# Performance work log

Measured on AMD Instinct MI355X. Metric: run time of the kernel, lower is better.

## Reference

```python
import jax, jax.numpy as jnp
import numpy as np

TOP_K = 2  # num_experts_per_tok


def setup_inputs() -> dict:
    key = jax.random.key(0)
    k1, k2, k3, k4, k5 = jax.random.split(key, 5)
    B, S, D, F, E = 2, 1024, 1024, 2048, 8
    return {
        "x": jax.random.normal(k1, (B, S, D), dtype=jnp.float32),
        "router_kernel_DE": jax.random.normal(k2, (D, E), dtype=jnp.float32) * 0.02,
        "kernel_gating_EDF": jax.random.normal(k3, (E, D, F), dtype=jnp.float32) * 0.02,
        "kernel_up_EDF": jax.random.normal(k4, (E, D, F), dtype=jnp.float32) * 0.02,
        "kernel_down_EFD": jax.random.normal(k5, (E, F, D), dtype=jnp.float32) * 0.02,
    }


def reference(x, router_kernel_DE, kernel_gating_EDF, kernel_up_EDF, kernel_down_EFD):
    E = router_kernel_DE.shape[-1]
    x = x.astype(jnp.float32)
    # --- Router ---
    logits_BSE = jnp.einsum('BSD,DE->BSE', x, router_kernel_DE)
    probs_BSE = jax.nn.softmax(logits_BSE.astype(jnp.float32), axis=-1)
    weights_BSK, indices_BSK = jax.lax.top_k(probs_BSE, TOP_K)
    norm_weights_BSK = jax.nn.softmax(weights_BSK, axis=-1)
    # scatter top-k weights into dense [B,S,E]
    one_hot_BSKE = jax.nn.one_hot(indices_BSK, num_classes=E, dtype=x.dtype)
    full_weights_BSE = jnp.sum(one_hot_BSKE * norm_weights_BSK[..., None], axis=2)
    # --- Dense-over-all-experts MoE forward ---
    gating_BSEF = jnp.einsum('BSD,EDF->BSEF', x, kernel_gating_EDF)
    act_BSEF = jax.nn.silu(gating_BSEF)
    up_BSEF = jnp.einsum('BSD,EDF->BSEF', x, kernel_up_EDF)
    fuse_BSEF = act_BSEF * up_BSEF
    down_BSED = jnp.einsum('BSEF,EFD->BSED', fuse_BSEF, kernel_down_EFD)
    out_BSD = jnp.einsum('BSED,BSE->BSD', down_BSED, full_weights_BSE)
    return out_BSD.astype(jnp.float32)
```

## Files before the change

### kernel.cpp

```cpp
#include <hip/hip_runtime.h>
#include <hip/hip_bf16.h>
#include <stdint.h>

#define T_TOK 2048
#define DIM 1024
#define FDIM 2048
#define NEXP 8
#define NSLOT 4096
#define MAXTILE 64

typedef short bf16x8 __attribute__((ext_vector_type(8)));
typedef float f32x4 __attribute__((ext_vector_type(4)));

__device__ __forceinline__ unsigned short f2bf(float f) {
  union { float f; unsigned int u; } v; v.f = f;
  unsigned int r = v.u + 0x7FFFu + ((v.u >> 16) & 1u);
  return (unsigned short)(r >> 16);
}

__device__ __forceinline__ void gld_lds16(const void* g, void* l) {
  __builtin_amdgcn_global_load_lds(
      (const __attribute__((address_space(1))) unsigned int*)g,
      (__attribute__((address_space(3))) unsigned int*)l, 16, 0, 0);
}

__global__ void router_kernel(const float* __restrict__ x, const float* __restrict__ rk,
                              int* __restrict__ counts, int* __restrict__ tok_e,
                              float* __restrict__ tok_w) {
  int w = threadIdx.x >> 6, lane = threadIdx.x & 63;
  int t = blockIdx.x * 4 + w;
  float acc[NEXP];
#pragma unroll
  for (int e = 0; e < NEXP; ++e) acc[e] = 0.f;
  const float4* xr = (const float4*)(x + (size_t)t * DIM);
#pragma unroll
  for (int i = 0; i < 4; ++i) {
    float4 xv = xr[i * 64 + lane];
    int d0 = (i * 64 + lane) * 4;
#pragma unroll
    for (int j = 0; j < 4; ++j) {
      const float4* rr = (const float4*)(rk + (size_t)(d0 + j) * NEXP);
      float4 r0 = rr[0], r1 = rr[1];
      float xs = (j == 0) ? xv.x : (j == 1) ? xv.y : (j == 2) ? xv.z : xv.w;
      acc[0] += xs * r0.x; acc[1] += xs * r0.y; acc[2] += xs * r0.z; acc[3] += xs * r0.w;
      acc[4] += xs * r1.x; acc[5] += xs * r1.y; acc[6] += xs * r1.z; acc[7] += xs * r1.w;
    }
  }
#pragma unroll
  for (int off = 32; off > 0; off >>= 1) {
#pragma unroll
    for (int e = 0; e < NEXP; ++e) acc[e] += __shfl_xor(acc[e], off, 64);
  }
  if (lane == 0) {
    float m = acc[0];
    for (int e = 1; e < NEXP; ++e) m = fmaxf(m, acc[e]);
    float p[NEXP], s = 0.f;
    for (int e = 0; e < NEXP; ++e) { p[e] = expf(acc[e] - m); s += p[e]; }
    float inv = 1.f / s;
    for (int e = 0; e < NEXP; ++e) p[e] *= inv;
    int i1 = 0;
    for (int e = 1; e < NEXP; ++e) if (p[e] > p[i1]) i1 = e;
    int i2 = (i1 == 0) ? 1 : 0;
    for (int e = 0; e < NEXP; ++e) if (e != i1 && p[e] > p[i2]) i2 = e;
    float e1 = expf(p[i1]), e2 = expf(p[i2]);
    float winv = 1.f / (e1 + e2);
    tok_e[t * 2] = i1; tok_e[t * 2 + 1] = i2;
    tok_w[t * 2] = e1 * winv; tok_w[t * 2 + 1] = e2 * winv;
    atomicAdd(&counts[i1], 1); atomicAdd(&counts[i2], 1);
  }
}

__global__ void scan_kernel(const int* __restrict__ counts, int* __restrict__ offsets,
                            int* __restrict__ tile_e, int* __restrict__ tile_mt,
                            int* __restrict__ ntiles) {
  if (threadIdx.x == 0) {
    int s = 0, t = 0;
    for (int e = 0; e < NEXP; ++e) {
      offsets[e] = s; s += counts[e];
      int nt = (counts[e] + 127) >> 7;
      for (int m = 0; m < nt; ++m) { tile_e[t] = e; tile_mt[t] = m; ++t; }
    }
    ntiles[0] = t;
  }
}

__global__ void assign_kernel(const int* __restrict__ tok_e, const float* __restrict__ tok_w,
                              const int* __restrict__ offsets, int* __restrict__ cursor,
                              int* __restrict__ slot_token, float* __restrict__ slot_weight,
                              int* __restrict__ tok_slot) {
  int t = blockIdx.x * 256 + threadIdx.x;
  if (t >= T_TOK) return;
#pragma unroll
  for (int k = 0; k < 2; ++k) {
    int e = tok_e[t * 2 + k];
    int pos = atomicAdd(&cursor[e], 1);
    int slot = offsets[e] + pos;
    slot_token[slot] = t;
    slot_weight[slot] = tok_w[t * 2 + k];
    tok_slot[t * 2 + k] = slot;
  }
}

__global__ void cvt_x_kernel(const float* __restrict__ x, unsigned short* __restrict__ xb) {
  int i = blockIdx.x * 256 + threadIdx.x;
  const float4* p = (const float4*)x;
  float4 a = p[i * 2], b = p[i * 2 + 1];
  uint4 o;
  o.x = ((unsigned)f2bf(a.y) << 16) | f2bf(a.x);
  o.y = ((unsigned)f2bf(a.w) << 16) | f2bf(a.z);
  o.z = ((unsigned)f2bf(b.y) << 16) | f2bf(b.x);
  o.w = ((unsigned)f2bf(b.w) << 16) | f2bf(b.z);
  ((uint4*)xb)[i] = o;
}

__global__ void transpose_cvt_kernel(const float* __restrict__ in, unsigned short* __restrict__ out,
                                     int R, int C) {
  __shared__ float lds[64][65];
  int e = blockIdx.z;
  size_t base = (size_t)e * (size_t)R * (size_t)C;
  int rb = blockIdx.y * 64, cb = blockIdx.x * 64;
  int tid = threadIdx.x;
  int col4 = (tid & 15) * 4, row = tid >> 4;
#pragma unroll
  for (int it = 0; it < 4; ++it) {
    int r = row + it * 16;
    float4 v = *(const float4*)(in + base + (size_t)(rb + r) * C + cb + col4);
    lds[col4 + 0][r] = v.x; lds[col4 + 1][r] = v.y;
    lds[col4 + 2][r] = v.z; lds[col4 + 3][r] = v.w;
  }
  __syncthreads();
  int r2 = (tid & 31) * 2, c = tid >> 5;
#pragma unroll
  for (int it = 0; it < 8; ++it) {
    int cc = c + it * 8;
    unsigned v = ((unsigned)f2bf(lds[cc][r2 + 1]) << 16) | f2bf(lds[cc][r2]);
    *(unsigned*)(out + base + (size_t)(cb + cc) * R + rb + r2) = v;
  }
}


__global__ __launch_bounds__(256) void gemm_gateup(
    const unsigned short* __restrict__ xb, const unsigned short* __restrict__ wg,
    const unsigned short* __restrict__ wu, const int* __restrict__ counts,
    const int* __restrict__ offsets, const int* __restrict__ slot_token,
    const int* __restrict__ tile_e, const int* __restrict__ tile_mt,
    const int* __restrict__ ntiles, unsigned short* __restrict__ fuse) {
  int ys = blockIdx.y;
  if (ys >= ntiles[0]) return;
  int e = tile_e[ys], mt = tile_mt[ys];
  int cnt = counts[e];
  int off = offsets[e];
  int nt = blockIdx.x;
  __shared__ unsigned short Al[128 * 64];
  __shared__ unsigned short Bgl[128 * 64];
  __shared__ unsigned short Bul[128 * 64];
  int tid = threadIdx.x, w = tid >> 6, lane = tid & 63;
  int w4 = w * 4;
  int csrc = ((lane & 7) ^ (lane >> 3)) * 8;
  const unsigned short* asrc[4];
  const unsigned short* bgsrc[4];
  const unsigned short* busrc[4];
#pragma unroll
  for (int ii = 0; ii < 4; ++ii) {
    int i = w4 + ii;
    int r = i * 8 + (lane >> 3);
    int row = mt * 128 + r;
    int tok = (row < cnt) ? slot_token[off + row] : 0;
    asrc[ii] = xb + (size_t)tok * DIM + csrc;
    size_t frow = (size_t)e * FDIM + (size_t)(nt * 128 + r);
    bgsrc[ii] = wg + frow * DIM + csrc;
    busrc[ii] = wu + frow * DIM + csrc;
  }
  f32x4 accg[4][4] = {};
  f32x4 accu[4][4] = {};
  int wr = (w >> 1) * 64, wc = (w & 1) * 64;
  int swz = (lane & 7) << 3;
  int kof0 = ((lane >> 4) * 8) ^ swz;
  int kof1 = (32 + (lane >> 4) * 8) ^ swz;
  for (int k0 = 0; k0 < DIM; k0 += 64) {
#pragma unroll
    for (int ii = 0; ii < 4; ++ii) {
      int i = w4 + ii;
      gld_lds16(asrc[ii] + k0, &Al[i * 512]);
      gld_lds16(bgsrc[ii] + k0, &Bgl[i * 512]);
      gld_lds16(busrc[ii] + k0, &Bul[i * 512]);
    }
    __syncthreads();
#pragma unroll
    for (int kk = 0; kk < 2; ++kk) {
      int kof = kk ? kof1 : kof0;
      bf16x8 af[4], bg[4], bu[4];
#pragma unroll
      for (int q = 0; q < 4; ++q) {
        af[q] = *(const bf16x8*)&Al[(wr + q * 16 + (lane & 15)) * 64 + kof];
        bg[q] = *(const bf16x8*)&Bgl[(wc + q * 16 + (lane & 15)) * 64 + kof];
        bu[q] = *(const bf16x8*)&Bul[(wc + q * 16 + (lane & 15)) * 64 + kof];
      }
#pragma unroll
      for (int m4 = 0; m4 < 4; ++m4) {
#pragma unroll
        for (int n4 = 0; n4 < 4; ++n4) {
          accg[m4][n4] = __builtin_amdgcn_mfma_f32_16x16x32_bf16(af[m4], bg[n4], accg[m4][n4], 0, 0, 0);
          accu[m4][n4] = __builtin_amdgcn_mfma_f32_16x16x32_bf16(af[m4], bu[n4], accu[m4][n4], 0, 0, 0);
        }
      }
    }
    __syncthreads();
  }
#pragma unroll
  for (int m4 = 0; m4 < 4; ++m4) {
#pragma unroll
    for (int n4 = 0; n4 < 4; ++n4) {
      f32x4 g = accg[m4][n4], u = accu[m4][n4];
#pragma unroll
      for (int j = 0; j < 4; ++j) {
        int r = wr + m4 * 16 + (lane >> 4) * 4 + j;
        int row = mt * 128 + r;
        if (row < cnt) {
          float gv = g[j];
          float val = gv / (1.f + expf(-gv)) * u[j];
          int f = nt * 128 + wc + n4 * 16 + (lane & 15);
          fuse[(size_t)(off + row) * FDIM + f] = f2bf(val);
        }
      }
    }
  }
}

__global__ __launch_bounds__(256) void gemm_down(
    const unsigned short* __restrict__ fuse, const unsigned short* __restrict__ wd,
    const int* __restrict__ counts, const int* __restrict__ offsets,
    const float* __restrict__ slot_weight, const int* __restrict__ tile_e,
    const int* __restrict__ tile_mt, const int* __restrict__ ntiles,
    float* __restrict__ part) {
  int ys = blockIdx.y;
  if (ys >= ntiles[0]) return;
  int e = tile_e[ys], mt = tile_mt[ys];
  int cnt = counts[e];
  int off = offsets[e];
  int nt = blockIdx.x;
  __shared__ unsigned short Al[128 * 64];
  __shared__ unsigned short Bl[128 * 64];
  int tid = threadIdx.x, w = tid >> 6, lane = tid & 63;
  int w4 = w * 4;
  int csrc = ((lane & 7) ^ (lane >> 3)) * 8;
  const unsigned short* asrc[4];
  const unsigned short* bsrc[4];
#pragma unroll
  for (int ii = 0; ii < 4; ++ii) {
    int i = w4 + ii;
    int r = i * 8 + (lane >> 3);
    int row = mt * 128 + r;
    int grow = (row < cnt) ? (off + row) : off;
    asrc[ii] = fuse + (size_t)grow * FDIM + csrc;
    size_t drow = (size_t)e * DIM + (size_t)(nt * 128 + r);
    bsrc[ii] = wd + drow * FDIM + csrc;
  }
  f32x4 acc[4][4] = {};
  int wr = (w >> 1) * 64, wc = (w & 1) * 64;
  int swz = (lane & 7) << 3;
  int kof0 = ((lane >> 4) * 8) ^ swz;
  int kof1 = (32 + (lane >> 4) * 8) ^ swz;
  for (int k0 = 0; k0 < FDIM; k0 += 64) {
#pragma unroll
    for (int ii = 0; ii < 4; ++ii) {
      int i = w4 + ii;
      gld_lds16(asrc[ii] + k0, &Al[i * 512]);
      gld_lds16(bsrc[ii] + k0, &Bl[i * 512]);
    }
    __syncthreads();
#pragma unroll
    for (int kk = 0; kk < 2; ++kk) {
      int kof = kk ? kof1 : kof0;
      bf16x8 af[4], bfr[4];
#pragma unroll
      for (int q = 0; q < 4; ++q) {
        af[q] = *(const bf16x8*)&Al[(wr + q * 16 + (lane & 15)) * 64 + kof];
        bfr[q] = *(const bf16x8*)&Bl[(wc + q * 16 + (lane & 15)) * 64 + kof];
      }
#pragma unroll
      for (int m4 = 0; m4 < 4; ++m4) {
#pragma unroll
        for (int n4 = 0; n4 < 4; ++n4) {
          acc[m4][n4] = __builtin_amdgcn_mfma_f32_16x16x32_bf16(af[m4], bfr[n4], acc[m4][n4], 0, 0, 0);
        }
      }
    }
    __syncthreads();
  }
#pragma unroll
  for (int m4 = 0; m4 < 4; ++m4) {
#pragma unroll
    for (int j = 0; j < 4; ++j) {
      int r = wr + m4 * 16 + (lane >> 4) * 4 + j;
      int row = mt * 128 + r;
      if (row < cnt) {
        float wgt = slot_weight[off + row];
#pragma unroll
        for (int n4 = 0; n4 < 4; ++n4) {
          int d = nt * 128 + wc + n4 * 16 + (lane & 15);
          part[(size_t)(off + row) * DIM + d] = acc[m4][n4][j] * wgt;
        }
      }
    }
  }
}

__global__ void combine_kernel(const float* __restrict__ part, const int* __restrict__ tok_slot,
                               float* __restrict__ out) {
  int i = blockIdx.x * 256 + threadIdx.x;
  int t = i >> 8;
  int c = i & 255;
  int s0 = tok_slot[t * 2], s1 = tok_slot[t * 2 + 1];
  float4 a = ((const float4*)(part + (size_t)s0 * DIM))[c];
  float4 b = ((const float4*)(part + (size_t)s1 * DIM))[c];
  float4 o;
  o.x = a.x + b.x; o.y = a.y + b.y; o.z = a.z + b.z; o.w = a.w + b.w;
  ((float4*)(out + (size_t)t * DIM))[c] = o;
}

extern "C" void kernel_launch(void* const* d_in, const int* in_sizes, int n_in,
                              void* d_out, int out_size, void* d_ws, size_t ws_size,
                              hipStream_t stream) {
  (void)in_sizes; (void)n_in; (void)out_size;
  const float* x    = (const float*)d_in[0];
  const float* rk   = (const float*)d_in[1];
  const float* wg_f = (const float*)d_in[2];
  const float* wu_f = (const float*)d_in[3];
  const float* wd_f = (const float*)d_in[4];
  float* out = (float*)d_out;

  char* ws = (char*)d_ws;
  size_t o_xb   = 0;
  size_t o_wg   = o_xb + (size_t)T_TOK * DIM * 2;
  size_t o_wu   = o_wg + (size_t)NEXP * FDIM * DIM * 2;
  size_t o_wd   = o_wu + (size_t)NEXP * FDIM * DIM * 2;
  size_t o_fuse = o_wd + (size_t)NEXP * DIM * FDIM * 2;
  size_t o_part = o_fuse + (size_t)NSLOT * FDIM * 2;
  size_t o_meta = o_part + (size_t)NSLOT * DIM * 4;
  size_t o_counts = o_meta;
  size_t o_cursor = o_counts + 32;
  size_t o_offs   = o_cursor + 32;
  size_t o_tok_e  = o_offs + 32;
  size_t o_tok_w  = o_tok_e + (size_t)T_TOK * 2 * 4;
  size_t o_tok_s  = o_tok_w + (size_t)T_TOK * 2 * 4;
  size_t o_st     = o_tok_s + (size_t)T_TOK * 2 * 4;
  size_t o_sw     = o_st + (size_t)NSLOT * 4;
  size_t o_te     = o_sw + (size_t)NSLOT * 4;
  size_t o_tm     = o_te + MAXTILE * 4;
  size_t o_ntl    = o_tm + MAXTILE * 4;
  size_t need     = o_ntl + 32;
  if (ws_size < need) return;

  unsigned short* xb   = (unsigned short*)(ws + o_xb);
  unsigned short* wgt  = (unsigned short*)(ws + o_wg);
  unsigned short* wut  = (unsigned short*)(ws + o_wu);
  unsigned short* wdt  = (unsigned short*)(ws + o_wd);
  unsigned short* fuse = (unsigned short*)(ws + o_fuse);
  float* part          = (float*)(ws + o_part);
  int* counts          = (int*)(ws + o_counts);
  int* cursor          = (int*)(ws + o_cursor);
  int* offsets         = (int*)(ws + o_offs);
  int* tok_e           = (int*)(ws + o_tok_e);
  float* tok_w         = (float*)(ws + o_tok_w);
  int* tok_slot        = (int*)(ws + o_tok_s);
  int* slot_token      = (int*)(ws + o_st);
  float* slot_weight   = (float*)(ws + o_sw);
  int* tile_e          = (int*)(ws + o_te);
  int* tile_mt         = (int*)(ws + o_tm);
  int* ntiles          = (int*)(ws + o_ntl);

  hipMemsetAsync(ws + o_counts, 0, 64, stream);
  router_kernel<<<T_TOK / 4, 256, 0, stream>>>(x, rk, counts, tok_e, tok_w);
  scan_kernel<<<1, 64, 0, stream>>>(counts, offsets, tile_e, tile_mt, ntiles);
  assign_kernel<<<T_TOK / 256, 256, 0, stream>>>(tok_e, tok_w, offsets, cursor,
                                                 slot_token, slot_weight, tok_slot);
  cvt_x_kernel<<<(T_TOK * DIM / 8) / 256, 256, 0, stream>>>(x, xb);
  transpose_cvt_kernel<<<dim3(FDIM / 64, DIM / 64, NEXP), 256, 0, stream>>>(wg_f, wgt, DIM, FDIM);
  transpose_cvt_kernel<<<dim3(FDIM / 64, DIM / 64, NEXP), 256, 0, stream>>>(wu_f, wut, DIM, FDIM);
  transpose_cvt_kernel<<<dim3(DIM / 64, FDIM / 64, NEXP), 256, 0, stream>>>(wd_f, wdt, FDIM, DIM);
  gemm_gateup<<<dim3(FDIM / 128, MAXTILE * 40 / 64, 1), 256, 0, stream>>>(
      xb, wgt, wut, counts, offsets, slot_token, tile_e, tile_mt, ntiles, fuse);
  gemm_down<<<dim3(DIM / 128, MAXTILE * 40 / 64, 1), 256, 0, stream>>>(
      fuse, wdt, counts, offsets, slot_weight, tile_e, tile_mt, ntiles, part);
  combine_kernel<<<(T_TOK * DIM / 4) / 256, 256, 0, stream>>>(part, tok_slot, out);
}
```

Measured before the change: 290.4 us.

## Narrow GEMM N-tiles, split-K the down projection, store partials in bf16

Halves the N tile width of both expert GEMMs from 128 to 64 and splits the down-projection K dimension into two halves via a z grid dimension. The goal is more workgroups to fill the GPU's compute units and better occupancy through launch bounds hints. Split-K partials are written as bf16 into a doubled buffer and summed in the combine kernel, which now reads four bf16 vectors per output. Narrower tiles cut arithmetic intensity and re-read the A tile more often, and bf16 partials add rounding error.

```diff
diff --git a/kernel.cpp b/kernel.cpp
--- a/kernel.cpp
+++ b/kernel.cpp
@@ -10,12 +10,18 @@
 #define MAXTILE 64
 
 typedef short bf16x8 __attribute__((ext_vector_type(8)));
+typedef unsigned short u16x8 __attribute__((ext_vector_type(8)));
 typedef float f32x4 __attribute__((ext_vector_type(4)));
 
 __device__ __forceinline__ unsigned short f2bf(float f) {
   union { float f; unsigned int u; } v; v.f = f;
   unsigned int r = v.u + 0x7FFFu + ((v.u >> 16) & 1u);
   return (unsigned short)(r >> 16);
+}
+
+__device__ __forceinline__ float bf2f(unsigned short x) {
+  union { unsigned int u; float f; } v; v.u = ((unsigned int)x) << 16;
+  return v.f;
 }
 
 __device__ __forceinline__ void gld_lds16(const void* g, void* l) {
@@ -139,7 +145,7 @@
 }
 
 
-__global__ __launch_bounds__(256) void gemm_gateup(
+__global__ __launch_bounds__(256, 4) void gemm_gateup(
     const unsigned short* __restrict__ xb, const unsigned short* __restrict__ wg,
     const unsigned short* __restrict__ wu, const int* __restrict__ counts,
     const int* __restrict__ offsets, const int* __restrict__ slot_token,
@@ -152,54 +158,59 @@
   int off = offsets[e];
   int nt = blockIdx.x;
   __shared__ unsigned short Al[128 * 64];
-  __shared__ unsigned short Bgl[128 * 64];
-  __shared__ unsigned short Bul[128 * 64];
+  __shared__ unsigned short Bgl[64 * 64];
+  __shared__ unsigned short Bul[64 * 64];
   int tid = threadIdx.x, w = tid >> 6, lane = tid & 63;
-  int w4 = w * 4;
   int csrc = ((lane & 7) ^ (lane >> 3)) * 8;
   const unsigned short* asrc[4];
-  const unsigned short* bgsrc[4];
-  const unsigned short* busrc[4];
+  const unsigned short* bgsrc[2];
+  const unsigned short* busrc[2];
 #pragma unroll
   for (int ii = 0; ii < 4; ++ii) {
-    int i = w4 + ii;
-    int r = i * 8 + (lane >> 3);
+    int r = (w * 4 + ii) * 8 + (lane >> 3);
     int row = mt * 128 + r;
     int tok = (row < cnt) ? slot_token[off + row] : 0;
     asrc[ii] = xb + (size_t)tok * DIM + csrc;
-    size_t frow = (size_t)e * FDIM + (size_t)(nt * 128 + r);
+  }
+#pragma unroll
+  for (int ii = 0; ii < 2; ++ii) {
+    int r = (w * 2 + ii) * 8 + (lane >> 3);
+    size_t frow = (size_t)e * FDIM + (size_t)(nt * 64 + r);
     bgsrc[ii] = wg + frow * DIM + csrc;
     busrc[ii] = wu + frow * DIM + csrc;
   }
-  f32x4 accg[4][4] = {};
-  f32x4 accu[4][4] = {};
-  int wr = (w >> 1) * 64, wc = (w & 1) * 64;
+  f32x4 accg[4][2] = {};
+  f32x4 accu[4][2] = {};
+  int wr = (w >> 1) * 64, wc = (w & 1) * 32;
   int swz = (lane & 7) << 3;
   int kof0 = ((lane >> 4) * 8) ^ swz;
   int kof1 = (32 + (lane >> 4) * 8) ^ swz;
   for (int k0 = 0; k0 < DIM; k0 += 64) {
 #pragma unroll
-    for (int ii = 0; ii < 4; ++ii) {
-      int i = w4 + ii;
-      gld_lds16(asrc[ii] + k0, &Al[i * 512]);
-      gld_lds16(bgsrc[ii] + k0, &Bgl[i * 512]);
-      gld_lds16(busrc[ii] + k0, &Bul[i * 512]);
+    for (int ii = 0; ii < 4; ++ii)
+      gld_lds16(asrc[ii] + k0, &Al[(w * 4 + ii) * 512]);
+#pragma unroll
+    for (int ii = 0; ii < 2; ++ii) {
+      gld_lds16(bgsrc[ii] + k0, &Bgl[(w * 2 + ii) * 512]);
+      gld_lds16(busrc[ii] + k0, &Bul[(w * 2 + ii) * 512]);
     }
     __syncthreads();
 #pragma unroll
     for (int kk = 0; kk < 2; ++kk) {
       int kof = kk ? kof1 : kof0;
-      bf16x8 af[4], bg[4], bu[4];
-#pragma unroll
-      for (int q = 0; q < 4; ++q) {
+      bf16x8 af[4], bg[2], bu[2];
+#pragma unroll
+      for (int q = 0; q < 4; ++q)
         af[q] = *(const bf16x8*)&Al[(wr + q * 16 + (lane & 15)) * 64 + kof];
+#pragma unroll
+      for (int q = 0; q < 2; ++q) {
         bg[q] = *(const bf16x8*)&Bgl[(wc + q * 16 + (lane & 15)) * 64 + kof];
         bu[q] = *(const bf16x8*)&Bul[(wc + q * 16 + (lane & 15)) * 64 + kof];
       }
 #pragma unroll
       for (int m4 = 0; m4 < 4; ++m4) {
 #pragma unroll
-        for (int n4 = 0; n4 < 4; ++n4) {
+        for (int n4 = 0; n4 < 2; ++n4) {
           accg[m4][n4] = __builtin_amdgcn_mfma_f32_16x16x32_bf16(af[m4], bg[n4], accg[m4][n4], 0, 0, 0);
           accu[m4][n4] = __builtin_amdgcn_mfma_f32_16x16x32_bf16(af[m4], bu[n4], accu[m4][n4], 0, 0, 0);
         }
@@ -210,7 +221,7 @@
 #pragma unroll
   for (int m4 = 0; m4 < 4; ++m4) {
 #pragma unroll
-    for (int n4 = 0; n4 < 4; ++n4) {
+    for (int n4 = 0; n4 < 2; ++n4) {
       f32x4 g = accg[m4][n4], u = accu[m4][n4];
 #pragma unroll
       for (int j = 0; j < 4; ++j) {
@@ -219,7 +230,7 @@
         if (row < cnt) {
           float gv = g[j];
           float val = gv / (1.f + expf(-gv)) * u[j];
-          int f = nt * 128 + wc + n4 * 16 + (lane & 15);
+          int f = nt * 64 + wc + n4 * 16 + (lane & 15);
           fuse[(size_t)(off + row) * FDIM + f] = f2bf(val);
         }
       }
@@ -227,61 +238,66 @@
   }
 }
 
-__global__ __launch_bounds__(256) void gemm_down(
+__global__ __launch_bounds__(256, 4) void gemm_down(
     const unsigned short* __restrict__ fuse, const unsigned short* __restrict__ wd,
     const int* __restrict__ counts, const int* __restrict__ offsets,
     const float* __restrict__ slot_weight, const int* __restrict__ tile_e,
     const int* __restrict__ tile_mt, const int* __restrict__ ntiles,
-    float* __restrict__ part) {
+    unsigned short* __restrict__ part2) {
   int ys = blockIdx.y;
   if (ys >= ntiles[0]) return;
   int e = tile_e[ys], mt = tile_mt[ys];
   int cnt = counts[e];
   int off = offsets[e];
   int nt = blockIdx.x;
+  int z = blockIdx.z;
+  int kbase = z * (FDIM / 2);
   __shared__ unsigned short Al[128 * 64];
-  __shared__ unsigned short Bl[128 * 64];
+  __shared__ unsigned short Bl[64 * 64];
   int tid = threadIdx.x, w = tid >> 6, lane = tid & 63;
-  int w4 = w * 4;
   int csrc = ((lane & 7) ^ (lane >> 3)) * 8;
   const unsigned short* asrc[4];
-  const unsigned short* bsrc[4];
+  const unsigned short* bsrc[2];
 #pragma unroll
   for (int ii = 0; ii < 4; ++ii) {
-    int i = w4 + ii;
-    int r = i * 8 + (lane >> 3);
+    int r = (w * 4 + ii) * 8 + (lane >> 3);
     int row = mt * 128 + r;
     int grow = (row < cnt) ? (off + row) : off;
-    asrc[ii] = fuse + (size_t)grow * FDIM + csrc;
-    size_t drow = (size_t)e * DIM + (size_t)(nt * 128 + r);
-    bsrc[ii] = wd + drow * FDIM + csrc;
-  }
-  f32x4 acc[4][4] = {};
-  int wr = (w >> 1) * 64, wc = (w & 1) * 64;
+    asrc[ii] = fuse + (size_t)grow * FDIM + kbase + csrc;
+  }
+#pragma unroll
+  for (int ii = 0; ii < 2; ++ii) {
+    int r = (w * 2 + ii) * 8 + (lane >> 3);
+    size_t drow = (size_t)e * DIM + (size_t)(nt * 64 + r);
+    bsrc[ii] = wd + drow * FDIM + kbase + csrc;
+  }
+  f32x4 acc[4][2] = {};
+  int wr = (w >> 1) * 64, wc = (w & 1) * 32;
   int swz = (lane & 7) << 3;
   int kof0 = ((lane >> 4) * 8) ^ swz;
   int kof1 = (32 + (lane >> 4) * 8) ^ swz;
-  for (int k0 = 0; k0 < FDIM; k0 += 64) {
-#pragma unroll
-    for (int ii = 0; ii < 4; ++ii) {
-      int i = w4 + ii;
-      gld_lds16(asrc[ii] + k0, &Al[i * 512]);
-      gld_lds16(bsrc[ii] + k0, &Bl[i * 512]);
-    }
+  for (int k0 = 0; k0 < FDIM / 2; k0 += 64) {
+#pragma unroll
+    for (int ii = 0; ii < 4; ++ii)
+      gld_lds16(asrc[ii] + k0, &Al[(w * 4 + ii) * 512]);
+#pragma unroll
+    for (int ii = 0; ii < 2; ++ii)
+      gld_lds16(bsrc[ii] + k0, &Bl[(w * 2 + ii) * 512]);
     __syncthreads();
 #pragma unroll
     for (int kk = 0; kk < 2; ++kk) {
       int kof = kk ? kof1 : kof0;
-      bf16x8 af[4], bfr[4];
-#pragma unroll
-      for (int q = 0; q < 4; ++q) {
+      bf16x8 af[4], bfr[2];
+#pragma unroll
+      for (int q = 0; q < 4; ++q)
         af[q] = *(const bf16x8*)&Al[(wr + q * 16 + (lane & 15)) * 64 + kof];
+#pragma unroll
+      for (int q = 0; q < 2; ++q)
         bfr[q] = *(const bf16x8*)&Bl[(wc + q * 16 + (lane & 15)) * 64 + kof];
-      }
 #pragma unroll
       for (int m4 = 0; m4 < 4; ++m4) {
 #pragma unroll
-        for (int n4 = 0; n4 < 4; ++n4) {
+        for (int n4 = 0; n4 < 2; ++n4) {
           acc[m4][n4] = __builtin_amdgcn_mfma_f32_16x16x32_bf16(af[m4], bfr[n4], acc[m4][n4], 0, 0, 0);
         }
       }
@@ -297,26 +313,33 @@
       if (row < cnt) {
         float wgt = slot_weight[off + row];
 #pragma unroll
-        for (int n4 = 0; n4 < 4; ++n4) {
-          int d = nt * 128 + wc + n4 * 16 + (lane & 15);
-          part[(size_t)(off + row) * DIM + d] = acc[m4][n4][j] * wgt;
+        for (int n4 = 0; n4 < 2; ++n4) {
+          int d = nt * 64 + wc + n4 * 16 + (lane & 15);
+          part2[((size_t)z * NSLOT + off + row) * DIM + d] = f2bf(acc[m4][n4][j] * wgt);
         }
       }
     }
   }
 }
 
-__global__ void combine_kernel(const float* __restrict__ part, const int* __restrict__ tok_slot,
-                               float* __restrict__ out) {
+__global__ void combine_kernel(const unsigned short* __restrict__ part2,
+                               const int* __restrict__ tok_slot, float* __restrict__ out) {
   int i = blockIdx.x * 256 + threadIdx.x;
-  int t = i >> 8;
-  int c = i & 255;
+  int t = i >> 7;
+  int c = i & 127;
   int s0 = tok_slot[t * 2], s1 = tok_slot[t * 2 + 1];
-  float4 a = ((const float4*)(part + (size_t)s0 * DIM))[c];
-  float4 b = ((const float4*)(part + (size_t)s1 * DIM))[c];
-  float4 o;
-  o.x = a.x + b.x; o.y = a.y + b.y; o.z = a.z + b.z; o.w = a.w + b.w;
-  ((float4*)(out + (size_t)t * DIM))[c] = o;
+  const u16x8* base = (const u16x8*)part2;
+  u16x8 a0 = base[((size_t)s0) * (DIM / 8) + c];
+  u16x8 a1 = base[((size_t)NSLOT + s0) * (DIM / 8) + c];
+  u16x8 b0 = base[((size_t)s1) * (DIM / 8) + c];
+  u16x8 b1 = base[((size_t)NSLOT + s1) * (DIM / 8) + c];
+  float o[8];
+#pragma unroll
+  for (int j = 0; j < 8; ++j)
+    o[j] = (bf2f(a0[j]) + bf2f(a1[j])) + (bf2f(b0[j]) + bf2f(b1[j]));
+  float4* dst = (float4*)(out + (size_t)t * DIM + c * 8);
+  dst[0] = make_float4(o[0], o[1], o[2], o[3]);
+  dst[1] = make_float4(o[4], o[5], o[6], o[7]);
 }
 
 extern "C" void kernel_launch(void* const* d_in, const int* in_sizes, int n_in,
@@ -337,7 +360,7 @@
   size_t o_wd   = o_wu + (size_t)NEXP * FDIM * DIM * 2;
   size_t o_fuse = o_wd + (size_t)NEXP * DIM * FDIM * 2;
   size_t o_part = o_fuse + (size_t)NSLOT * FDIM * 2;
-  size_t o_meta = o_part + (size_t)NSLOT * DIM * 4;
+  size_t o_meta = o_part + (size_t)2 * NSLOT * DIM * 2;
   size_t o_counts = o_meta;
   size_t o_cursor = o_counts + 32;
   size_t o_offs   = o_cursor + 32;
@@ -352,12 +375,12 @@
   size_t need     = o_ntl + 32;
   if (ws_size < need) return;
 
-  unsigned short* xb   = (unsigned short*)(ws + o_xb);
-  unsigned short* wgt  = (unsigned short*)(ws + o_wg);
-  unsigned short* wut  = (unsigned short*)(ws + o_wu);
-  unsigned short* wdt  = (unsigned short*)(ws + o_wd);
-  unsigned short* fuse = (unsigned short*)(ws + o_fuse);
-  float* part          = (float*)(ws + o_part);
+  unsigned short* xb    = (unsigned short*)(ws + o_xb);
+  unsigned short* wgt   = (unsigned short*)(ws + o_wg);
+  unsigned short* wut   = (unsigned short*)(ws + o_wu);
+  unsigned short* wdt   = (unsigned short*)(ws + o_wd);
+  unsigned short* fuse  = (unsigned short*)(ws + o_fuse);
+  unsigned short* part2 = (unsigned short*)(ws + o_part);
   int* counts          = (int*)(ws + o_counts);
   int* cursor          = (int*)(ws + o_cursor);
   int* offsets         = (int*)(ws + o_offs);
@@ -379,9 +402,10 @@
   transpose_cvt_kernel<<<dim3(FDIM / 64, DIM / 64, NEXP), 256, 0, stream>>>(wg_f, wgt, DIM, FDIM);
   transpose_cvt_kernel<<<dim3(FDIM / 64, DIM / 64, NEXP), 256, 0, stream>>>(wu_f, wut, DIM, FDIM);
   transpose_cvt_kernel<<<dim3(DIM / 64, FDIM / 64, NEXP), 256, 0, stream>>>(wd_f, wdt, FDIM, DIM);
-  gemm_gateup<<<dim3(FDIM / 128, MAXTILE * 40 / 64, 1), 256, 0, stream>>>(
+
+  gemm_gateup<<<dim3(FDIM / 64, 40, 1), 256, 0, stream>>>(
       xb, wgt, wut, counts, offsets, slot_token, tile_e, tile_mt, ntiles, fuse);
-  gemm_down<<<dim3(DIM / 128, MAXTILE * 40 / 64, 1), 256, 0, stream>>>(
-      fuse, wdt, counts, offsets, slot_weight, tile_e, tile_mt, ntiles, part);
-  combine_kernel<<<(T_TOK * DIM / 4) / 256, 256, 0, stream>>>(part, tok_slot, out);
-}
+  gemm_down<<<dim3(DIM / 64, 40, 2), 256, 0, stream>>>(
+      fuse, wdt, counts, offsets, slot_weight, tile_e, tile_mt, ntiles, part2);
+  combine_kernel<<<(T_TOK * DIM / 8) / 256, 256, 0, stream>>>(part2, tok_slot, out);
+}
```

Measured after the change: 325.2 us. 1.12x slower.
